# Kernel tuning notes

Hardware: AMD Instinct MI355X
Metric: run time of the kernel (lower is better)

The kernel has to match this reference:

```python
import jax, jax.numpy as jnp
import numpy as np

N_HEADS = 16
ROPE_DIMS = 16
SEQ_LEN = 512


def _rope_cache(T, dtype=jnp.float32):
    rd = ROPE_DIMS
    freqs = 1.0 / (10000.0 ** (jnp.arange(0, rd, 2, dtype=jnp.float32) / rd))  # [rd/2]
    t = jnp.arange(T, dtype=jnp.float32)
    ang = jnp.outer(t, freqs)  # [T, rd/2]
    return jnp.cos(ang).astype(dtype), jnp.sin(ang).astype(dtype)


def _apply_rope(x, cos, sin):
    # x: [B, H, T, hd]; partial RoPE on first ROPE_DIMS dims
    rd = ROPE_DIMS
    x_rope, x_pass = x[..., :rd], x[..., rd:]
    x1, x2 = x_rope[..., : rd // 2], x_rope[..., rd // 2 :]
    # cos/sin: [T, rd/2] -> broadcast over B, H
    out = jnp.concatenate([x1 * cos - x2 * sin, x2 * cos + x1 * sin], axis=-1)
    return jnp.concatenate([out, x_pass], axis=-1)


def setup_inputs() -> dict:
    key = jax.random.key(0)
    k1, k2, k3 = jax.random.split(key, 3)
    B, T, C = 8, SEQ_LEN, 2048
    x = jax.random.normal(k1, (B, T, C), dtype=jnp.float32)
    Wqkv = jax.random.normal(k2, (3 * C, C), dtype=jnp.float32) * (1.0 / np.sqrt(C))
    Wout = jax.random.normal(k3, (C, C), dtype=jnp.float32) * (1.0 / np.sqrt(C))
    return {"x": x, "Wqkv": Wqkv, "Wout": Wout}


def reference(x, Wqkv, Wout):
    B, T, C = x.shape
    H = N_HEADS
    hd = C // H
    # fused QKV projection
    qkv = jnp.einsum("btc,fc->btf", x, Wqkv)  # [B, T, 3C]
    qkv = qkv.reshape(B, T, 3, H, hd)
    q, k, v = qkv[:, :, 0], qkv[:, :, 1], qkv[:, :, 2]  # [B, T, H, hd]
    q = jnp.transpose(q, (0, 2, 1, 3))  # [B, H, T, hd]
    k = jnp.transpose(k, (0, 2, 1, 3))
    v = jnp.transpose(v, (0, 2, 1, 3))
    cos, sin = _rope_cache(T, dtype=x.dtype)
    q = _apply_rope(q, cos, sin)
    k = _apply_rope(k, cos, sin)
    # causal SDPA
    scale = 1.0 / np.sqrt(hd)
    scores = jnp.einsum("bhqd,bhkd->bhqk", q, k) * scale
    causal = jnp.tril(jnp.ones((T, T), dtype=bool))
    scores = jnp.where(causal, scores, jnp.finfo(scores.dtype).min)
    attn = jax.nn.softmax(scores, axis=-1)
    y = jnp.einsum("bhqk,bhkd->bhqd", attn, v)  # [B, H, T, hd]
    y = jnp.transpose(y, (0, 2, 1, 3)).reshape(B, T, C)
    return jnp.einsum("btc,oc->bto", y, Wout)
```

## Files before the change

kernel.cpp:

```cpp
#include <hip/hip_runtime.h>

typedef __bf16 bf16_t;
typedef __bf16 bf16x4 __attribute__((ext_vector_type(4)));
typedef __bf16 bf16x8 __attribute__((ext_vector_type(8)));
typedef float f32x4 __attribute__((ext_vector_type(4)));

#define GLB(p) ((const __attribute__((address_space(1))) void*)(p))
#define LDS(p) ((__attribute__((address_space(3))) void*)(p))

__global__ void f32_to_bf16(const float* __restrict__ src, bf16_t* __restrict__ dst, int n8)
{
    const int i = blockIdx.x * 256 + threadIdx.x;
    if (i >= n8) return;
    const f32x4 a = *(const f32x4*)&src[(size_t)i * 8];
    const f32x4 b = *(const f32x4*)&src[(size_t)i * 8 + 4];
    bf16x8 h = {(bf16_t)a[0], (bf16_t)a[1], (bf16_t)a[2], (bf16_t)a[3],
                (bf16_t)b[0], (bf16_t)b[1], (bf16_t)b[2], (bf16_t)b[3]};
    *(bf16x8*)&dst[(size_t)i * 8] = h;
}

#define LDB4(d, kk)                                                            \
    { _Pragma("unroll") for (int nt = 0; nt < 4; ++nt)                         \
        bfr[nt] = *(const bf16x8*)&smem[sBe + (d) * 32768 + (kk) * 8192 + nt * 512]; }

#define LDA4(d, kk, g)                                                         \
    { _Pragma("unroll") for (int i = 0; i < 4; ++i)                            \
        afr[i] = *(const bf16x8*)&smem[sAe + (d) * 32768 + (kk) * 8192 + ((g) * 4 + i) * 512]; }

#define MM4(g)                                                                 \
    { _Pragma("unroll") for (int i = 0; i < 4; ++i)                            \
        _Pragma("unroll") for (int nt = 0; nt < 4; ++nt)                       \
            acc[(g) * 4 + i][nt] = __builtin_amdgcn_mfma_f32_16x16x32_bf16(    \
                afr[i], bfr[nt], acc[(g) * 4 + i][nt], 0, 0, 0); }

#define PHASE_TAIL(g)                                                          \
    __builtin_amdgcn_s_barrier();                                              \
    asm volatile("s_waitcnt lgkmcnt(0)" ::: "memory");                         \
    __builtin_amdgcn_s_setprio(1);                                             \
    MM4(g);                                                                    \
    __builtin_amdgcn_s_setprio(0);                                             \
    __builtin_amdgcn_s_barrier();

template <int MODE>
__global__ __launch_bounds__(512, 2)
void gemm256(const bf16_t* __restrict__ A, const bf16_t* __restrict__ Bm, int K,
             bf16_t* __restrict__ o0, bf16_t* __restrict__ o1, bf16_t* __restrict__ o2,
             float* __restrict__ of)
{
    __shared__ __align__(16) bf16_t smem[65536];

    const int tid  = threadIdx.x;
    const int lane = tid & 63;
    const int w    = tid >> 6;
    const int wr   = w >> 2;
    const int wc   = w & 3;
    const int quad = lane >> 4;
    const int qcol = lane & 15;
    const int m0   = blockIdx.x * 256;
    const int n0   = blockIdx.y * 256;

    f32x4 acc[8][4];
#pragma unroll
    for (int i = 0; i < 8; ++i)
#pragma unroll
        for (int j = 0; j < 4; ++j)
            acc[i][j] = (f32x4){0.f, 0.f, 0.f, 0.f};

    const int srow = w * 16 + (lane >> 2);
    const int scg  = (lane & 3) ^ ((lane >> 3) & 3);
    const bf16_t* Ag = A  + (size_t)(m0 + srow) * K + scg * 8;
    const bf16_t* Bg = Bm + (size_t)(n0 + srow) * K + scg * 8;

    auto STAGE = [&](int d, int t, int hh) {
        const int isA = hh & 1;
        const int kh  = hh >> 1;
        const bf16_t* g = (isA ? Ag : Bg) + t * 64 + kh * 32;
        bf16_t* l = &smem[d * 32768 + kh * 8192 + (isA ? 0 : 16384) + w * 512];
        __builtin_amdgcn_global_load_lds(GLB(g), LDS(l), 16, 0, 0);
        __builtin_amdgcn_global_load_lds(GLB(g + (size_t)128 * K), LDS(l + 4096), 16, 0, 0);
    };

    const int rs8 = (quad ^ ((qcol >> 1) & 3)) * 8;
    const int sAe = (wr * 128 + qcol) * 32 + rs8;
    const int sBe = 16384 + (wc * 64 + qcol) * 32 + rs8;

    bf16x8 afr[4], bfr[4];

    const int NT  = K >> 6;
    const int NIT = NT >> 1;

    STAGE(0, 0, 0); STAGE(0, 0, 1); STAGE(0, 0, 2); STAGE(0, 0, 3);
    STAGE(1, 1, 0); STAGE(1, 1, 1); STAGE(1, 1, 2);
    asm volatile("s_waitcnt vmcnt(6)" ::: "memory");
    __builtin_amdgcn_s_barrier();

    for (int J = 0; J < NIT - 1; ++J) {
        const int t = 2 * J;
        LDB4(0, 0); LDA4(0, 0, 0); STAGE(1, t + 1, 3);
        PHASE_TAIL(0);
        LDA4(0, 0, 1); STAGE(0, t + 2, 0);
        PHASE_TAIL(1);
        LDB4(0, 1); LDA4(0, 1, 0); STAGE(0, t + 2, 1);
        PHASE_TAIL(0);
        LDA4(0, 1, 1); STAGE(0, t + 2, 2);
        asm volatile("s_waitcnt vmcnt(6)" ::: "memory");
        PHASE_TAIL(1);
        LDB4(1, 0); LDA4(1, 0, 0); STAGE(0, t + 2, 3);
        PHASE_TAIL(0);
        LDA4(1, 0, 1); STAGE(1, t + 3, 0);
        PHASE_TAIL(1);
        LDB4(1, 1); LDA4(1, 1, 0); STAGE(1, t + 3, 1);
        PHASE_TAIL(0);
        LDA4(1, 1, 1); STAGE(1, t + 3, 2);
        asm volatile("s_waitcnt vmcnt(6)" ::: "memory");
        PHASE_TAIL(1);
    }

    {
        const int t = NT - 2;
        LDB4(0, 0); LDA4(0, 0, 0); STAGE(1, t + 1, 3);
        PHASE_TAIL(0);
        LDA4(0, 0, 1);
        PHASE_TAIL(1);
        LDB4(0, 1); LDA4(0, 1, 0);
        PHASE_TAIL(0);
        LDA4(0, 1, 1);
        asm volatile("s_waitcnt vmcnt(0)" ::: "memory");
        PHASE_TAIL(1);
        LDB4(1, 0); LDA4(1, 0, 0);
        PHASE_TAIL(0);
        LDA4(1, 0, 1);
        PHASE_TAIL(1);
        LDB4(1, 1); LDA4(1, 1, 0);
        PHASE_TAIL(0);
        LDA4(1, 1, 1);
        __builtin_amdgcn_s_barrier();
        asm volatile("s_waitcnt lgkmcnt(0)" ::: "memory");
        __builtin_amdgcn_s_setprio(1);
        MM4(1);
        __builtin_amdgcn_s_setprio(0);
    }

#pragma unroll
    for (int mt = 0; mt < 8; ++mt) {
#pragma unroll
        for (int nt = 0; nt < 4; ++nt) {
#pragma unroll
            for (int r = 0; r < 4; ++r) {
                const int m = m0 + wr * 128 + mt * 16 + quad * 4 + r;
                const int f = n0 + wc * 64 + nt * 16 + qcol;
                const float val = acc[mt][nt][r];
                if (MODE == 0) {
                    const int b     = m >> 9;
                    const int t     = m & 511;
                    const int which = f >> 11;
                    const int h     = (f >> 7) & 15;
                    const int d     = f & 127;
                    if (which == 2) {
                        o2[((size_t)(((b << 4) + h) * 128 + d) << 9) + t] = (bf16_t)val;
                    } else {
                        bf16_t* dst = (which == 0) ? o0 : o1;
                        dst[(size_t)(((b << 4) + h) * 512 + t) * 128 + d] = (bf16_t)val;
                    }
                } else {
                    of[(size_t)m * 2048 + f] = val;
                }
            }
        }
    }
}

__global__ void rope_kernel(bf16_t* __restrict__ q, bf16_t* __restrict__ k)
{
    const int id  = blockIdx.x * 256 + threadIdx.x;
    const int arr = id >> 19;
    const int rem = id & ((1 << 19) - 1);
    const int bh  = rem >> 12;
    const int t   = (rem >> 3) & 511;
    const int d   = rem & 7;

    bf16_t* p = (arr ? k : q) + (size_t)(bh * 512 + t) * 128;
    const float x1 = (float)p[d];
    const float x2 = (float)p[d + 8];
    const float freq = __expf(-(float)d * 1.1512925464970229f);
    const float ang  = (float)t * freq;
    const float c = cosf(ang), s = sinf(ang);
    p[d]     = (bf16_t)(x1 * c - x2 * s);
    p[d + 8] = (bf16_t)(x2 * c + x1 * s);
}

#define KLD 136
#define VLD 72
#define PLD 72

__global__ __launch_bounds__(256)
void flash_attn(const bf16_t* __restrict__ q, const bf16_t* __restrict__ k,
                const bf16_t* __restrict__ vT, bf16_t* __restrict__ y)
{
    const int qtb = blockIdx.x;
    const int h   = blockIdx.y;
    const int b   = blockIdx.z;
    const int tid  = threadIdx.x;
    const int lane = tid & 63;
    const int w    = tid >> 6;
    const int quad = lane >> 4;
    const int qcol = lane & 15;

    __shared__ __align__(16) bf16_t Ks[64 * KLD];
    __shared__ __align__(16) bf16_t VTs[128 * VLD];
    __shared__ __align__(16) bf16_t Ps[128 * PLD];
    __shared__ __align__(16) float aS[4][2][16];
    __shared__ __align__(16) float lS[4][2][16];

    const bf16_t* qb  = q  + (size_t)((b * 16 + h) * 512) * 128;
    const bf16_t* kb  = k  + (size_t)((b * 16 + h) * 512) * 128;
    const bf16_t* vtb = vT + (size_t)((b * 16 + h) * 128) * 512;

    bf16x8 qfrag[2][4];
#pragma unroll
    for (int qg = 0; qg < 2; ++qg) {
        const int qrow = qtb * 128 + w * 32 + qg * 16 + qcol;
#pragma unroll
        for (int kc = 0; kc < 4; ++kc)
            qfrag[qg][kc] = *(const bf16x8*)&qb[(size_t)qrow * 128 + kc * 32 + quad * 8];
    }

    f32x4 acc_o[2][8];
#pragma unroll
    for (int qg = 0; qg < 2; ++qg)
#pragma unroll
        for (int nt = 0; nt < 8; ++nt) acc_o[qg][nt] = (f32x4){0.f, 0.f, 0.f, 0.f};
    float m_run[2] = {-INFINITY, -INFINITY};
    float l_run[2] = {0.f, 0.f};
    const float scale = 0.08838834764831845f;

    const int kt_last = 2 * qtb + 1;
    for (int kt = 0; kt <= kt_last; ++kt) {
        __syncthreads();
#pragma unroll
        for (int p = 0; p < 4; ++p) {
            const int r = p * 16 + (tid >> 4), c = (tid & 15) * 8;
            *(uint4*)&Ks[r * KLD + c] = *(const uint4*)&kb[(size_t)(kt * 64 + r) * 128 + c];
        }
#pragma unroll
        for (int p = 0; p < 4; ++p) {
            const int r = p * 32 + (tid >> 3), c = (tid & 7) * 8;
            *(uint4*)&VTs[r * VLD + c] = *(const uint4*)&vtb[(size_t)r * 512 + kt * 64 + c];
        }
        __syncthreads();

        const bool need_mask = (kt >= 2 * qtb);

#pragma unroll
        for (int qg = 0; qg < 2; ++qg) {
            f32x4 sacc[4];
#pragma unroll
            for (int mt = 0; mt < 4; ++mt) sacc[mt] = (f32x4){0.f, 0.f, 0.f, 0.f};
#pragma unroll
            for (int mt = 0; mt < 4; ++mt)
#pragma unroll
                for (int kc = 0; kc < 4; ++kc) {
                    bf16x8 af = *(const bf16x8*)&Ks[(mt * 16 + qcol) * KLD + kc * 32 + quad * 8];
                    sacc[mt] = __builtin_amdgcn_mfma_f32_16x16x32_bf16(af, qfrag[qg][kc], sacc[mt], 0, 0, 0);
                }

            float s[16];
#pragma unroll
            for (int mt = 0; mt < 4; ++mt)
#pragma unroll
                for (int r = 0; r < 4; ++r)
                    s[mt * 4 + r] = sacc[mt][r] * scale;
            if (need_mask) {
                const int qglob = qtb * 128 + w * 32 + qg * 16 + qcol;
#pragma unroll
                for (int mt = 0; mt < 4; ++mt)
#pragma unroll
                    for (int r = 0; r < 4; ++r)
                        if (kt * 64 + mt * 16 + quad * 4 + r > qglob)
                            s[mt * 4 + r] = -1e30f;
            }

            float mx = s[0];
#pragma unroll
            for (int i = 1; i < 16; ++i) mx = fmaxf(mx, s[i]);
            mx = fmaxf(mx, __shfl_xor(mx, 16));
            mx = fmaxf(mx, __shfl_xor(mx, 32));
            const float m_new = fmaxf(m_run[qg], mx);
            const float alpha = __expf(m_run[qg] - m_new);
            float p16[16];
            float sum = 0.f;
#pragma unroll
            for (int i = 0; i < 16; ++i) { p16[i] = __expf(s[i] - m_new); sum += p16[i]; }
            sum += __shfl_xor(sum, 16);
            sum += __shfl_xor(sum, 32);
            l_run[qg] = l_run[qg] * alpha + sum;
            m_run[qg] = m_new;
            if (quad == 0) aS[w][qg][qcol] = alpha;

#pragma unroll
            for (int mt = 0; mt < 4; ++mt) {
                bf16x4 pb = {(bf16_t)p16[mt * 4 + 0], (bf16_t)p16[mt * 4 + 1],
                             (bf16_t)p16[mt * 4 + 2], (bf16_t)p16[mt * 4 + 3]};
                *(bf16x4*)&Ps[(w * 32 + qg * 16 + qcol) * PLD + mt * 16 + quad * 4] = pb;
            }

            f32x4 alpha4 = *(const f32x4*)&aS[w][qg][quad * 4];
#pragma unroll
            for (int nt = 0; nt < 8; ++nt)
#pragma unroll
                for (int r = 0; r < 4; ++r)
                    acc_o[qg][nt][r] *= alpha4[r];

#pragma unroll
            for (int kc2 = 0; kc2 < 2; ++kc2) {
                bf16x8 pf = *(const bf16x8*)&Ps[(w * 32 + qg * 16 + qcol) * PLD + kc2 * 32 + quad * 8];
#pragma unroll
                for (int nt = 0; nt < 8; ++nt) {
                    bf16x8 vf = *(const bf16x8*)&VTs[(nt * 16 + qcol) * VLD + kc2 * 32 + quad * 8];
                    acc_o[qg][nt] = __builtin_amdgcn_mfma_f32_16x16x32_bf16(pf, vf, acc_o[qg][nt], 0, 0, 0);
                }
            }
        }
    }

    if (quad == 0) { lS[w][0][qcol] = l_run[0]; lS[w][1][qcol] = l_run[1]; }
#pragma unroll
    for (int qg = 0; qg < 2; ++qg) {
        f32x4 l4 = *(const f32x4*)&lS[w][qg][quad * 4];
#pragma unroll
        for (int nt = 0; nt < 8; ++nt)
#pragma unroll
            for (int r = 0; r < 4; ++r) {
                const int t  = qtb * 128 + w * 32 + qg * 16 + quad * 4 + r;
                const int cc = h * 128 + nt * 16 + qcol;
                y[(size_t)(b * 512 + t) * 2048 + cc] = (bf16_t)(acc_o[qg][nt][r] / l4[r]);
            }
    }
}

extern "C" void kernel_launch(void* const* d_in, const int* in_sizes, int n_in,
                              void* d_out, int out_size, void* d_ws, size_t ws_size,
                              hipStream_t stream)
{
    (void)in_sizes; (void)n_in; (void)out_size; (void)ws_size;

    const float* x    = (const float*)d_in[0];
    const float* Wqkv = (const float*)d_in[1];
    const float* Wout = (const float*)d_in[2];
    float* out = (float*)d_out;

    const size_t SEG = (size_t)8 * 16 * 512 * 128;
    bf16_t* q      = (bf16_t*)d_ws;
    bf16_t* k      = q + SEG;
    bf16_t* vT     = k + SEG;
    bf16_t* xb     = vT + SEG;
    bf16_t* y      = xb;
    bf16_t* Wqkvb  = xb + SEG;
    bf16_t* Woutb  = Wqkvb + (size_t)6144 * 2048;

    f32_to_bf16<<<(8388608 / 8) / 256, 256, 0, stream>>>(x, xb, 8388608 / 8);
    f32_to_bf16<<<(12582912 / 8) / 256, 256, 0, stream>>>(Wqkv, Wqkvb, 12582912 / 8);
    f32_to_bf16<<<(4194304 / 8) / 256, 256, 0, stream>>>(Wout, Woutb, 4194304 / 8);
    gemm256<0><<<dim3(4096 / 256, 6144 / 256), 512, 0, stream>>>(xb, Wqkvb, 2048, q, k, vT, nullptr);
    rope_kernel<<<(2 * 128 * 512 * 8) / 256, 256, 0, stream>>>(q, k);
    flash_attn<<<dim3(4, 16, 8), 256, 0, stream>>>(q, k, vT, y);
    gemm256<1><<<dim3(4096 / 256, 2048 / 256), 512, 0, stream>>>(y, Woutb, 2048, nullptr, nullptr, nullptr, out);
}
```

Baseline: 364.3 us.

## Enlarge flash-attention query tile to 256 rows and double-buffer GEMM fragments

Flash attention now processes 256 query rows per block (64 per wave), so each loaded K/V tile is reused across more queries and the grid is halved. The GEMM keeps two sets of A/B fragment registers, alternating between them across phases so loads for the next phase can overlap the current MFMAs. The larger attention tile raises register use and LDS footprint and reduces block count and causal load balance.

```diff
diff --git a/kernel.cpp b/kernel.cpp
--- a/kernel.cpp
+++ b/kernel.cpp
@@ -19,25 +19,25 @@
     *(bf16x8*)&dst[(size_t)i * 8] = h;
 }
 
-#define LDB4(d, kk)                                                            \
+#define LDB4(d, kk, S)                                                         \
     { _Pragma("unroll") for (int nt = 0; nt < 4; ++nt)                         \
-        bfr[nt] = *(const bf16x8*)&smem[sBe + (d) * 32768 + (kk) * 8192 + nt * 512]; }
-
-#define LDA4(d, kk, g)                                                         \
+        bfr[S][nt] = *(const bf16x8*)&smem[sBe + (d) * 32768 + (kk) * 8192 + nt * 512]; }
+
+#define LDA4(d, kk, g, S)                                                      \
     { _Pragma("unroll") for (int i = 0; i < 4; ++i)                            \
-        afr[i] = *(const bf16x8*)&smem[sAe + (d) * 32768 + (kk) * 8192 + ((g) * 4 + i) * 512]; }
-
-#define MM4(g)                                                                 \
+        afr[S][i] = *(const bf16x8*)&smem[sAe + (d) * 32768 + (kk) * 8192 + ((g) * 4 + i) * 512]; }
+
+#define MM4(g, SA, SB)                                                         \
     { _Pragma("unroll") for (int i = 0; i < 4; ++i)                            \
         _Pragma("unroll") for (int nt = 0; nt < 4; ++nt)                       \
             acc[(g) * 4 + i][nt] = __builtin_amdgcn_mfma_f32_16x16x32_bf16(    \
-                afr[i], bfr[nt], acc[(g) * 4 + i][nt], 0, 0, 0); }
-
-#define PHASE_TAIL(g)                                                          \
+                afr[SA][i], bfr[SB][nt], acc[(g) * 4 + i][nt], 0, 0, 0); }
+
+#define PHASE_TAIL(g, SA, SB)                                                  \
     __builtin_amdgcn_s_barrier();                                              \
     asm volatile("s_waitcnt lgkmcnt(0)" ::: "memory");                         \
     __builtin_amdgcn_s_setprio(1);                                             \
-    MM4(g);                                                                    \
+    MM4(g, SA, SB);                                                            \
     __builtin_amdgcn_s_setprio(0);                                             \
     __builtin_amdgcn_s_barrier();
 
@@ -84,7 +84,7 @@
     const int sAe = (wr * 128 + qcol) * 32 + rs8;
     const int sBe = 16384 + (wc * 64 + qcol) * 32 + rs8;
 
-    bf16x8 afr[4], bfr[4];
+    bf16x8 afr[2][4], bfr[2][4];
 
     const int NT  = K >> 6;
     const int NIT = NT >> 1;
@@ -96,48 +96,48 @@
 
     for (int J = 0; J < NIT - 1; ++J) {
         const int t = 2 * J;
-        LDB4(0, 0); LDA4(0, 0, 0); STAGE(1, t + 1, 3);
-        PHASE_TAIL(0);
-        LDA4(0, 0, 1); STAGE(0, t + 2, 0);
-        PHASE_TAIL(1);
-        LDB4(0, 1); LDA4(0, 1, 0); STAGE(0, t + 2, 1);
-        PHASE_TAIL(0);
-        LDA4(0, 1, 1); STAGE(0, t + 2, 2);
+        LDB4(0, 0, 0); LDA4(0, 0, 0, 0); STAGE(1, t + 1, 3);
+        PHASE_TAIL(0, 0, 0);
+        LDA4(0, 0, 1, 1); STAGE(0, t + 2, 0);
+        PHASE_TAIL(1, 1, 0);
+        LDB4(0, 1, 1); LDA4(0, 1, 0, 0); STAGE(0, t + 2, 1);
+        PHASE_TAIL(0, 0, 1);
+        LDA4(0, 1, 1, 1); STAGE(0, t + 2, 2);
         asm volatile("s_waitcnt vmcnt(6)" ::: "memory");
-        PHASE_TAIL(1);
-        LDB4(1, 0); LDA4(1, 0, 0); STAGE(0, t + 2, 3);
-        PHASE_TAIL(0);
-        LDA4(1, 0, 1); STAGE(1, t + 3, 0);
-        PHASE_TAIL(1);
-        LDB4(1, 1); LDA4(1, 1, 0); STAGE(1, t + 3, 1);
-        PHASE_TAIL(0);
-        LDA4(1, 1, 1); STAGE(1, t + 3, 2);
+        PHASE_TAIL(1, 1, 1);
+        LDB4(1, 0, 0); LDA4(1, 0, 0, 0); STAGE(0, t + 2, 3);
+        PHASE_TAIL(0, 0, 0);
+        LDA4(1, 0, 1, 1); STAGE(1, t + 3, 0);
+        PHASE_TAIL(1, 1, 0);
+        LDB4(1, 1, 1); LDA4(1, 1, 0, 0); STAGE(1, t + 3, 1);
+        PHASE_TAIL(0, 0, 1);
+        LDA4(1, 1, 1, 1); STAGE(1, t + 3, 2);
         asm volatile("s_waitcnt vmcnt(6)" ::: "memory");
-        PHASE_TAIL(1);
+        PHASE_TAIL(1, 1, 1);
     }
 
     {
         const int t = NT - 2;
-        LDB4(0, 0); LDA4(0, 0, 0); STAGE(1, t + 1, 3);
-        PHASE_TAIL(0);
-        LDA4(0, 0, 1);
-        PHASE_TAIL(1);
-        LDB4(0, 1); LDA4(0, 1, 0);
-        PHASE_TAIL(0);
-        LDA4(0, 1, 1);
+        LDB4(0, 0, 0); LDA4(0, 0, 0, 0); STAGE(1, t + 1, 3);
+        PHASE_TAIL(0, 0, 0);
+        LDA4(0, 0, 1, 1);
+        PHASE_TAIL(1, 1, 0);
+        LDB4(0, 1, 1); LDA4(0, 1, 0, 0);
+        PHASE_TAIL(0, 0, 1);
+        LDA4(0, 1, 1, 1);
         asm volatile("s_waitcnt vmcnt(0)" ::: "memory");
-        PHASE_TAIL(1);
-        LDB4(1, 0); LDA4(1, 0, 0);
-        PHASE_TAIL(0);
-        LDA4(1, 0, 1);
-        PHASE_TAIL(1);
-        LDB4(1, 1); LDA4(1, 1, 0);
-        PHASE_TAIL(0);
-        LDA4(1, 1, 1);
+        PHASE_TAIL(1, 1, 1);
+        LDB4(1, 0, 0); LDA4(1, 0, 0, 0);
+        PHASE_TAIL(0, 0, 0);
+        LDA4(1, 0, 1, 1);
+        PHASE_TAIL(1, 1, 0);
+        LDB4(1, 1, 1); LDA4(1, 1, 0, 0);
+        PHASE_TAIL(0, 0, 1);
+        LDA4(1, 1, 1, 1);
         __builtin_amdgcn_s_barrier();
         asm volatile("s_waitcnt lgkmcnt(0)" ::: "memory");
         __builtin_amdgcn_s_setprio(1);
-        MM4(1);
+        MM4(1, 1, 1);
         __builtin_amdgcn_s_setprio(0);
     }
 
@@ -208,33 +208,33 @@
 
     __shared__ __align__(16) bf16_t Ks[64 * KLD];
     __shared__ __align__(16) bf16_t VTs[128 * VLD];
-    __shared__ __align__(16) bf16_t Ps[128 * PLD];
-    __shared__ __align__(16) float aS[4][2][16];
-    __shared__ __align__(16) float lS[4][2][16];
+    __shared__ __align__(16) bf16_t Ps[256 * PLD];
+    __shared__ __align__(16) float aS[4][4][16];
+    __shared__ __align__(16) float lS[4][4][16];
 
     const bf16_t* qb  = q  + (size_t)((b * 16 + h) * 512) * 128;
     const bf16_t* kb  = k  + (size_t)((b * 16 + h) * 512) * 128;
     const bf16_t* vtb = vT + (size_t)((b * 16 + h) * 128) * 512;
 
-    bf16x8 qfrag[2][4];
-#pragma unroll
-    for (int qg = 0; qg < 2; ++qg) {
-        const int qrow = qtb * 128 + w * 32 + qg * 16 + qcol;
+    bf16x8 qfrag[4][4];
+#pragma unroll
+    for (int qg = 0; qg < 4; ++qg) {
+        const int qrow = qtb * 256 + w * 64 + qg * 16 + qcol;
 #pragma unroll
         for (int kc = 0; kc < 4; ++kc)
             qfrag[qg][kc] = *(const bf16x8*)&qb[(size_t)qrow * 128 + kc * 32 + quad * 8];
     }
 
-    f32x4 acc_o[2][8];
-#pragma unroll
-    for (int qg = 0; qg < 2; ++qg)
+    f32x4 acc_o[4][8];
+#pragma unroll
+    for (int qg = 0; qg < 4; ++qg)
 #pragma unroll
         for (int nt = 0; nt < 8; ++nt) acc_o[qg][nt] = (f32x4){0.f, 0.f, 0.f, 0.f};
-    float m_run[2] = {-INFINITY, -INFINITY};
-    float l_run[2] = {0.f, 0.f};
+    float m_run[4] = {-INFINITY, -INFINITY, -INFINITY, -INFINITY};
+    float l_run[4] = {0.f, 0.f, 0.f, 0.f};
     const float scale = 0.08838834764831845f;
 
-    const int kt_last = 2 * qtb + 1;
+    const int kt_last = 4 * qtb + 3;
     for (int kt = 0; kt <= kt_last; ++kt) {
         __syncthreads();
 #pragma unroll
@@ -249,10 +249,10 @@
         }
         __syncthreads();
 
-        const bool need_mask = (kt >= 2 * qtb);
-
-#pragma unroll
-        for (int qg = 0; qg < 2; ++qg) {
+        const bool need_mask = (kt >= 4 * qtb);
+
+#pragma unroll
+        for (int qg = 0; qg < 4; ++qg) {
             f32x4 sacc[4];
 #pragma unroll
             for (int mt = 0; mt < 4; ++mt) sacc[mt] = (f32x4){0.f, 0.f, 0.f, 0.f};
@@ -271,7 +271,7 @@
                 for (int r = 0; r < 4; ++r)
                     s[mt * 4 + r] = sacc[mt][r] * scale;
             if (need_mask) {
-                const int qglob = qtb * 128 + w * 32 + qg * 16 + qcol;
+                const int qglob = qtb * 256 + w * 64 + qg * 16 + qcol;
 #pragma unroll
                 for (int mt = 0; mt < 4; ++mt)
 #pragma unroll
@@ -301,7 +301,7 @@
             for (int mt = 0; mt < 4; ++mt) {
                 bf16x4 pb = {(bf16_t)p16[mt * 4 + 0], (bf16_t)p16[mt * 4 + 1],
                              (bf16_t)p16[mt * 4 + 2], (bf16_t)p16[mt * 4 + 3]};
-                *(bf16x4*)&Ps[(w * 32 + qg * 16 + qcol) * PLD + mt * 16 + quad * 4] = pb;
+                *(bf16x4*)&Ps[(w * 64 + qg * 16 + qcol) * PLD + mt * 16 + quad * 4] = pb;
             }
 
             f32x4 alpha4 = *(const f32x4*)&aS[w][qg][quad * 4];
@@ -313,7 +313,7 @@
 
 #pragma unroll
             for (int kc2 = 0; kc2 < 2; ++kc2) {
-                bf16x8 pf = *(const bf16x8*)&Ps[(w * 32 + qg * 16 + qcol) * PLD + kc2 * 32 + quad * 8];
+                bf16x8 pf = *(const bf16x8*)&Ps[(w * 64 + qg * 16 + qcol) * PLD + kc2 * 32 + quad * 8];
 #pragma unroll
                 for (int nt = 0; nt < 8; ++nt) {
                     bf16x8 vf = *(const bf16x8*)&VTs[(nt * 16 + qcol) * VLD + kc2 * 32 + quad * 8];
@@ -323,15 +323,18 @@
         }
     }
 
-    if (quad == 0) { lS[w][0][qcol] = l_run[0]; lS[w][1][qcol] = l_run[1]; }
-#pragma unroll
-    for (int qg = 0; qg < 2; ++qg) {
+    if (quad == 0) {
+#pragma unroll
+        for (int qg = 0; qg < 4; ++qg) lS[w][qg][qcol] = l_run[qg];
+    }
+#pragma unroll
+    for (int qg = 0; qg < 4; ++qg) {
         f32x4 l4 = *(const f32x4*)&lS[w][qg][quad * 4];
 #pragma unroll
         for (int nt = 0; nt < 8; ++nt)
 #pragma unroll
             for (int r = 0; r < 4; ++r) {
-                const int t  = qtb * 128 + w * 32 + qg * 16 + quad * 4 + r;
+                const int t  = qtb * 256 + w * 64 + qg * 16 + quad * 4 + r;
                 const int cc = h * 128 + nt * 16 + qcol;
                 y[(size_t)(b * 512 + t) * 2048 + cc] = (bf16_t)(acc_o[qg][nt][r] / l4[r]);
             }
@@ -363,6 +366,6 @@
     f32_to_bf16<<<(4194304 / 8) / 256, 256, 0, stream>>>(Wout, Woutb, 4194304 / 8);
     gemm256<0><<<dim3(4096 / 256, 6144 / 256), 512, 0, stream>>>(xb, Wqkvb, 2048, q, k, vT, nullptr);
     rope_kernel<<<(2 * 128 * 512 * 8) / 256, 256, 0, stream>>>(q, k);
-    flash_attn<<<dim3(4, 16, 8), 256, 0, stream>>>(q, k, vT, y);
+    flash_attn<<<dim3(2, 16, 8), 256, 0, stream>>>(q, k, vT, y);
     gemm256<1><<<dim3(4096 / 256, 2048 / 256), 512, 0, stream>>>(y, Woutb, 2048, nullptr, nullptr, nullptr, out);
 }
```

Result: slower. 373.7 us (+2.6%).
